# Kernel optimization log

Measured on AMD Instinct MI355X. Metric: run time of the kernel, lower is better.

The kernel has to match this reference:

```python
import jax, jax.numpy as jnp
import numpy as np

K = 5  # kernel_size per dim (dim=2 -> 25 kernels), B-spline degree 1, open spline


def spline_conv(x, edge_index, pseudo, W, root, bias):
    # x: [N, Cin], pseudo: [E, 2] in [0,1], W: [K*K, Cin, Cout]
    N = x.shape[0]
    src, dst = edge_index[0], edge_index[1]
    # Transform node features with every kernel weight once: [N, K*K, Cout]
    xk = jnp.einsum('ni,kio->nko', x, W)
    # Degree-1 open B-spline basis: v = u*(K-1); frac/1-frac weights over 2 knots per dim
    v = pseudo * (K - 1)
    bot = jnp.floor(v)
    frac = v - bot
    bot = bot.astype(jnp.int32)
    msg = jnp.zeros((src.shape[0], W.shape[2]), dtype=x.dtype)
    for s0 in (0, 1):
        for s1 in (0, 1):
            b0 = frac[:, 0] if s0 else (1.0 - frac[:, 0])
            b1 = frac[:, 1] if s1 else (1.0 - frac[:, 1])
            basis = b0 * b1  # [E]
            idx = (jnp.clip(bot[:, 0] + s0, 0, K - 1)
                   + K * jnp.clip(bot[:, 1] + s1, 0, K - 1))  # [E]
            msg = msg + basis[:, None] * xk[src, idx]  # gather [E, Cout]
    # scatter-max aggregation into target nodes; empty nodes -> 0 (PyG convention)
    agg = jax.ops.segment_max(msg, dst, num_segments=N)
    agg = jnp.where(jnp.isfinite(agg), agg, jnp.zeros_like(agg))
    return agg + x @ root + bias


def setup_inputs() -> dict:
    key = jax.random.key(0)
    ks = jax.random.split(key, 8)
    N, E, C = 50000, 1600000, 64
    Cin = C
    s = 1.0 / np.sqrt(25 * Cin)
    return {
        'x': jax.random.normal(ks[0], (N, C), dtype=jnp.float32),
        'edge_index': jax.random.randint(ks[1], (2, E), 0, N, dtype=jnp.int32),
        'edge_attr': jax.random.uniform(ks[2], (E, 2), dtype=jnp.float32),
        'W1': jax.random.normal(ks[3], (25, C, C), dtype=jnp.float32) * s,
        'root1': jax.random.normal(ks[4], (C, C), dtype=jnp.float32) / np.sqrt(C),
        'bias1': jnp.zeros((C,), dtype=jnp.float32),
        'W2': jax.random.normal(ks[5], (25, C, C), dtype=jnp.float32) * s,
        'root2': jax.random.normal(ks[6], (C, C), dtype=jnp.float32) / np.sqrt(C),
        'bias2': jnp.zeros((C,), dtype=jnp.float32),
    }


def reference(x, edge_index, edge_attr, W1, root1, bias1, W2, root2, bias2):
    h = jax.nn.relu(spline_conv(x, edge_index, edge_attr, W1, root1, bias1))
    out = spline_conv(h, edge_index, edge_attr, W2, root2, bias2)
    return out
```

## Files before the change

kernel.cpp:

```cpp
#include <hip/hip_runtime.h>
#include <hip/hip_bf16.h>
#include <math.h>

#define CHANNELS 64
#define KK 25
#define NBLK 26
#define NCOL (NBLK * CHANNELS)
#define NTILES (NCOL / 16)
#define ROWP 2560
#define GROUP_TILES 8
#define GROUP_BYTES (GROUP_TILES * 2048)
#define NGROUPS (NTILES / GROUP_TILES)

typedef __attribute__((ext_vector_type(8))) short bf16x8;
typedef __attribute__((ext_vector_type(4))) float f32x4;
typedef __attribute__((ext_vector_type(2))) float f32x2;
typedef unsigned int u32;

__device__ __forceinline__ u32 f2bfu(float f) {
    u32 u = __float_as_uint(f);
    return (u + 0x7FFFu + ((u >> 16) & 1u)) >> 16;
}
__device__ __forceinline__ short f2bf(float f) { return (short)f2bfu(f); }

__device__ __forceinline__ void async_copy16(const void* g, void* l) {
    __builtin_amdgcn_global_load_lds(
        (const __attribute__((address_space(1))) u32*)g,
        (__attribute__((address_space(3))) u32*)l, 16, 0, 0);
}


__global__ __launch_bounds__(256) void scan_a(const u32* __restrict__ counts,
                                              u32* __restrict__ bsum, int N) {
    const int t = threadIdx.x;
    const int base = blockIdx.x * 1024 + t * 4;
    uint4 v = make_uint4(0, 0, 0, 0);
    if (base + 3 < N) v = *(const uint4*)(counts + base);
    else {
        if (base < N)     v.x = counts[base];
        if (base + 1 < N) v.y = counts[base + 1];
        if (base + 2 < N) v.z = counts[base + 2];
    }
    u32 s = v.x + v.y + v.z + v.w;
    for (int off = 32; off; off >>= 1) s += __shfl_down(s, off, 64);
    __shared__ u32 red[4];
    if ((t & 63) == 0) red[t >> 6] = s;
    __syncthreads();
    if (t == 0) bsum[blockIdx.x] = red[0] + red[1] + red[2] + red[3];
}

__global__ __launch_bounds__(64) void scan_b(u32* __restrict__ bsum, int nb) {
    const int lane = threadIdx.x;
    u32 run = 0;
    for (int base = 0; base < nb; base += 64) {
        u32 v = (base + lane < nb) ? bsum[base + lane] : 0u;
        const u32 orig = v;
        for (int off = 1; off < 64; off <<= 1) {
            u32 u = __shfl_up(v, off, 64);
            if (lane >= off) v += u;
        }
        if (base + lane < nb) bsum[base + lane] = run + v - orig;
        run += __shfl(v, 63, 64);
    }
}

__global__ __launch_bounds__(256) void scan_c(const u32* __restrict__ counts,
                                              const u32* __restrict__ bsum,
                                              u32* __restrict__ cursor, int N) {
    const int t = threadIdx.x;
    const int base = blockIdx.x * 1024 + t * 4;
    uint4 v = make_uint4(0, 0, 0, 0);
    if (base + 3 < N) v = *(const uint4*)(counts + base);
    else {
        if (base < N)     v.x = counts[base];
        if (base + 1 < N) v.y = counts[base + 1];
        if (base + 2 < N) v.z = counts[base + 2];
    }
    __shared__ u32 ps[256];
    ps[t] = v.x + v.y + v.z + v.w;
    __syncthreads();
    for (int off = 1; off < 256; off <<= 1) {
        u32 u = (t >= off) ? ps[t - off] : 0u;
        __syncthreads();
        ps[t] += u;
        __syncthreads();
    }
    u32 ex = ((t > 0) ? ps[t - 1] : 0u) + bsum[blockIdx.x];
    if (base < N)     cursor[base]     = ex;
    if (base + 1 < N) cursor[base + 1] = ex + v.x;
    if (base + 2 < N) cursor[base + 2] = ex + v.x + v.y;
    if (base + 3 < N) cursor[base + 3] = ex + v.x + v.y + v.z;
    if (base <= N - 1 && N - 1 <= base + 3)
        cursor[N] = ex + v.x + v.y + v.z + v.w;
}


__global__ __launch_bounds__(256) void prep_w(const float* __restrict__ W,
                                              const float* __restrict__ root,
                                              __hip_bfloat16* __restrict__ Wb) {
    int idx = blockIdx.x * 256 + threadIdx.x;
    if (idx >= NTILES * 2 * 64 * 8) return;
    int j = idx & 7;
    int l = (idx >> 3) & 63;
    int q = (idx >> 9) & 1;
    int t = idx >> 10;
    int cell = t >> 2;
    int o    = 4 * (l & 15) + (t & 3);
    int k    = q * 32 + (l >> 4) * 8 + j;
    float src = (cell < KK) ? W[cell * 4096 + k * 64 + o] : root[k * 64 + o];
    ((unsigned short*)Wb)[idx] = (unsigned short)f2bf(src);
}

__device__ __forceinline__ void gemm_body(
    const float* __restrict__ X, const __hip_bfloat16* __restrict__ Wb,
    char* __restrict__ XK, float* __restrict__ rootf, int N, int gr0, int gr1)
{
    __shared__ __align__(16) char lds[2][GROUP_BYTES];
    const int lane = threadIdx.x & 63;
    const int wv   = threadIdx.x >> 6;
    const int rb   = blockIdx.x * 64 + wv * 16;
    const int m    = lane & 15;
    const int quad = lane >> 4;

    const int rowc = min(rb + m, N - 1);
    const float* __restrict__ xp = X + (size_t)rowc * CHANNELS + quad * 8;
    float af[16];
    *(float4*)(af)      = *(const float4*)(xp);
    *(float4*)(af + 4)  = *(const float4*)(xp + 4);
    *(float4*)(af + 8)  = *(const float4*)(xp + 32);
    *(float4*)(af + 12) = *(const float4*)(xp + 36);
    bf16x8 A0, A1;
#pragma unroll
    for (int j = 0; j < 8; ++j) { A0[j] = f2bf(af[j]); A1[j] = f2bf(af[8 + j]); }

    const int r0 = rb + quad * 4;
    const int rmax = N - r0;
    char* __restrict__ orow0 = XK + (size_t)r0 * ROWP;

    const char* __restrict__ wbc = (const char*)Wb;
#define STAGE(g, buf)                                                          \
    {                                                                          \
        const char* gsrc = wbc + (size_t)(g) * GROUP_BYTES + wv * 4096 + lane * 16; \
        char* lbase = lds[buf] + wv * 4096;                                    \
        async_copy16(gsrc,        lbase);                                      \
        async_copy16(gsrc + 1024, lbase + 1024);                               \
        async_copy16(gsrc + 2048, lbase + 2048);                               \
        async_copy16(gsrc + 3072, lbase + 3072);                               \
    }

    STAGE(gr0, 0)
    for (int g = gr0; g < gr1; ++g) {
        const int li = (g - gr0) & 1;
        __syncthreads();
        if (g + 1 < gr1) STAGE(g + 1, li ^ 1)
        const char* lb = lds[li] + lane * 16;
#pragma unroll
        for (int cc = 0; cc < 2; ++cc) {
            const char* cb = lb + cc * 8192;
            f32x4 acc0 = {0.f, 0.f, 0.f, 0.f};
            f32x4 acc1 = {0.f, 0.f, 0.f, 0.f};
            f32x4 acc2 = {0.f, 0.f, 0.f, 0.f};
            f32x4 acc3 = {0.f, 0.f, 0.f, 0.f};
            acc0 = __builtin_amdgcn_mfma_f32_16x16x32_bf16(A0, *(const bf16x8*)(cb),        acc0, 0, 0, 0);
            acc0 = __builtin_amdgcn_mfma_f32_16x16x32_bf16(A1, *(const bf16x8*)(cb + 1024), acc0, 0, 0, 0);
            acc1 = __builtin_amdgcn_mfma_f32_16x16x32_bf16(A0, *(const bf16x8*)(cb + 2048), acc1, 0, 0, 0);
            acc1 = __builtin_amdgcn_mfma_f32_16x16x32_bf16(A1, *(const bf16x8*)(cb + 3072), acc1, 0, 0, 0);
            acc2 = __builtin_amdgcn_mfma_f32_16x16x32_bf16(A0, *(const bf16x8*)(cb + 4096), acc2, 0, 0, 0);
            acc2 = __builtin_amdgcn_mfma_f32_16x16x32_bf16(A1, *(const bf16x8*)(cb + 5120), acc2, 0, 0, 0);
            acc3 = __builtin_amdgcn_mfma_f32_16x16x32_bf16(A0, *(const bf16x8*)(cb + 6144), acc3, 0, 0, 0);
            acc3 = __builtin_amdgcn_mfma_f32_16x16x32_bf16(A1, *(const bf16x8*)(cb + 7168), acc3, 0, 0, 0);
            const int kc = g * 2 + cc;
            if (kc < KK) {
                const int d1 = kc / 5;
                const int d0 = kc - 5 * d1;
                const int boff = d1 * 512 + d0 * 128 + 4 * m;
#pragma unroll
                for (int i = 0; i < 4; ++i) {
                    if (i < rmax) {
                        u32 p = __builtin_amdgcn_cvt_pk_fp8_f32(acc0[i], acc1[i], 0u, false);
                        p = __builtin_amdgcn_cvt_pk_fp8_f32(acc2[i], acc3[i], p, true);
                        char* orow = orow0 + (size_t)i * ROWP;
                        if (d0 <= 3) *(u32*)(orow + boff) = p;
                        if (d0 >= 1) *(u32*)(orow + boff - 64) = p;
                    }
                }
            } else {
#pragma unroll
                for (int i = 0; i < 4; ++i) {
                    if (i < rmax) {
                        *(float4*)(rootf + (size_t)(r0 + i) * CHANNELS + 4 * m) =
                            make_float4(acc0[i], acc1[i], acc2[i], acc3[i]);
                    }
                }
            }
        }
    }
#undef STAGE
}

__global__ __launch_bounds__(256) void gemm_hist(
    const float* __restrict__ X, const __hip_bfloat16* __restrict__ Wb,
    char* __restrict__ XK, float* __restrict__ rootf, int N, int gemm_blocks,
    const int* __restrict__ ei, u32* __restrict__ counts,
    u32* __restrict__ rank, int E)
{
    if ((int)blockIdx.x >= gemm_blocks) {
        const int e0 = ((int)blockIdx.x - gemm_blocks) * 1024 + threadIdx.x * 4;
        if (e0 + 3 < E) {
            const int4 d = *(const int4*)(ei + E + e0);
            const u32 r0 = atomicAdd(&counts[d.x], 1u);
            const u32 r1 = atomicAdd(&counts[d.y], 1u);
            const u32 r2 = atomicAdd(&counts[d.z], 1u);
            const u32 r3 = atomicAdd(&counts[d.w], 1u);
            *(uint4*)(rank + e0) = make_uint4(r0, r1, r2, r3);
        } else {
            for (int k = 0; k < 4; ++k)
                if (e0 + k < E)
                    rank[e0 + k] = atomicAdd(&counts[ei[E + e0 + k]], 1u);
        }
        return;
    }
    gemm_body(X, Wb, XK, rootf, N, 0, NGROUPS);
}

__global__ __launch_bounds__(256) void gemm_only(
    const float* __restrict__ X, const __hip_bfloat16* __restrict__ Wb,
    char* __restrict__ XK, float* __restrict__ rootf, int N)
{
    gemm_body(X, Wb, XK, rootf, N, 0, NGROUPS);
}

__device__ __forceinline__ uint2 mkrec(int src, float v0f, float v1f) {
    const float v0 = v0f * 4.0f, v1 = v1f * 4.0f;
    const int p0 = max(min((int)floorf(v0), 3), 0);
    const int p1 = max(min((int)floorf(v1), 3), 0);
    const float f0 = v0 - (float)p0;
    const float f1 = v1 - (float)p1;
    const u32 f0q = min((u32)(f0 * 65536.0f), 65535u);
    const u32 f1q = min((u32)(f1 * 65536.0f), 65535u);
    uint2 rec;
    rec.x = (u32)src | ((u32)p0 << 16) | ((u32)p1 << 19);
    rec.y = f0q | (f1q << 16);
    return rec;
}

__global__ __launch_bounds__(256) void edge_scatter(
    const int* __restrict__ ei, const float* __restrict__ ps,
    const u32* __restrict__ rank, const u32* __restrict__ cursor,
    uint2* __restrict__ sorted, int E)
{
    const int e0 = blockIdx.x * 1024 + threadIdx.x * 4;
    if (e0 + 3 < E) {
        const int4 s  = *(const int4*)(ei + e0);
        const int4 d  = *(const int4*)(ei + E + e0);
        const float4 pa = *(const float4*)(ps + 2 * e0);
        const float4 pb = *(const float4*)(ps + 2 * e0 + 4);
        const uint4 rk = *(const uint4*)(rank + e0);
        const u32 c0 = cursor[d.x];
        const u32 c1 = cursor[d.y];
        const u32 c2 = cursor[d.z];
        const u32 c3 = cursor[d.w];
        sorted[c0 + rk.x] = mkrec(s.x, pa.x, pa.y);
        sorted[c1 + rk.y] = mkrec(s.y, pa.z, pa.w);
        sorted[c2 + rk.z] = mkrec(s.z, pb.x, pb.y);
        sorted[c3 + rk.w] = mkrec(s.w, pb.z, pb.w);
    } else {
        for (int k = 0; k < 4; ++k) {
            const int e = e0 + k;
            if (e < E)
                sorted[cursor[ei[E + e]] + rank[e]] =
                    mkrec(ei[e], ps[2 * e], ps[2 * e + 1]);
        }
    }
}

__global__ __launch_bounds__(256) void agg_node_p(
    const uint2* __restrict__ sorted, const u32* __restrict__ cursor,
    const char* __restrict__ XK, const float* __restrict__ rootf,
    const float* __restrict__ bias, float* __restrict__ out, int N, int relu,
    int node_blocks, const float* __restrict__ Wsrc,
    const float* __restrict__ rootsrc, __hip_bfloat16* __restrict__ Wbdst)
{
    if ((int)blockIdx.x >= node_blocks) {
        int idx = ((int)blockIdx.x - node_blocks) * 256 + threadIdx.x;
        if (idx < NTILES * 2 * 64 * 8) {
            int j = idx & 7;
            int l = (idx >> 3) & 63;
            int q = (idx >> 9) & 1;
            int t = idx >> 10;
            int cell = t >> 2;
            int o    = 4 * (l & 15) + (t & 3);
            int k    = q * 32 + (l >> 4) * 8 + j;
            float s = (cell < KK) ? Wsrc[cell * 4096 + k * 64 + o] : rootsrc[k * 64 + o];
            ((unsigned short*)Wbdst)[idx] = (unsigned short)f2bf(s);
        }
        return;
    }
    const int lane = threadIdx.x & 63;
    const int n = blockIdx.x * 4 + (threadIdx.x >> 6);
    if (n >= N) return;
    const int q = lane >> 4, j = lane & 15;
    const int beg = (int)cursor[n];
    const int end = (int)cursor[n + 1];

    float m0 = -INFINITY, m1 = -INFINITY, m2 = -INFINITY, m3 = -INFINITY;
    if (beg < end) {
        const int last = end - 1;
#define GATHP(r, gll, ghl, glh, ghh)                                           \
        {                                                                      \
            const char* b_ = XK + (size_t)((r).x & 0xffff) * ROWP + (j << 2);  \
            const int o_ = (((int)((r).x >> 16) & 7)                           \
                            + (((int)((r).x >> 19) & 7) << 2)) << 7;           \
            gll = *(const u32*)(b_ + o_);                                      \
            ghl = *(const u32*)(b_ + o_ + 64);                                 \
            glh = *(const u32*)(b_ + o_ + 512);                                \
            ghh = *(const u32*)(b_ + o_ + 576);                                \
        }
        uint2 rA = sorted[min(beg + q,      last)];
        uint2 rB = sorted[min(beg + 4 + q,  last)];
        uint2 rC = sorted[min(beg + 8 + q,  last)];
        u32 a0, a1, a2, a3, b0, b1, b2, b3, c0, c1, c2, c3;
        GATHP(rA, a0, a1, a2, a3)
        GATHP(rB, b0, b1, b2, b3)
        for (int i = beg; i < end; i += 4) {
            uint2 rD = sorted[min(i + 12 + q, last)];
            GATHP(rC, c0, c1, c2, c3)
            const float f0 = (float)(rA.y & 0xffff) * (1.0f / 65536.0f);
            const float f1 = (float)(rA.y >> 16)    * (1.0f / 65536.0f);
            const float w00 = (1.f - f0) * (1.f - f1);
            const float w10 = f0 * (1.f - f1);
            const float w01 = (1.f - f0) * f1;
            const float w11 = f0 * f1;
            f32x2 s01 = __builtin_amdgcn_cvt_pk_f32_fp8(a0, false) * w00
                      + __builtin_amdgcn_cvt_pk_f32_fp8(a1, false) * w10
                      + __builtin_amdgcn_cvt_pk_f32_fp8(a2, false) * w01
                      + __builtin_amdgcn_cvt_pk_f32_fp8(a3, false) * w11;
            f32x2 s23 = __builtin_amdgcn_cvt_pk_f32_fp8(a0, true)  * w00
                      + __builtin_amdgcn_cvt_pk_f32_fp8(a1, true)  * w10
                      + __builtin_amdgcn_cvt_pk_f32_fp8(a2, true)  * w01
                      + __builtin_amdgcn_cvt_pk_f32_fp8(a3, true)  * w11;
            m0 = fmaxf(m0, s01.x); m1 = fmaxf(m1, s01.y);
            m2 = fmaxf(m2, s23.x); m3 = fmaxf(m3, s23.y);
            rA = rB; rB = rC; rC = rD;
            a0 = b0; a1 = b1; a2 = b2; a3 = b3;
            b0 = c0; b1 = c1; b2 = c2; b3 = c3;
        }
#undef GATHP
    }
    m0 = fmaxf(m0, __shfl_xor(m0, 16, 64)); m0 = fmaxf(m0, __shfl_xor(m0, 32, 64));
    m1 = fmaxf(m1, __shfl_xor(m1, 16, 64)); m1 = fmaxf(m1, __shfl_xor(m1, 32, 64));
    m2 = fmaxf(m2, __shfl_xor(m2, 16, 64)); m2 = fmaxf(m2, __shfl_xor(m2, 32, 64));
    m3 = fmaxf(m3, __shfl_xor(m3, 16, 64)); m3 = fmaxf(m3, __shfl_xor(m3, 32, 64));
    const float a0 = isfinite(m0) ? m0 : 0.f;
    const float a1 = isfinite(m1) ? m1 : 0.f;
    const float a2 = isfinite(m2) ? m2 : 0.f;
    const float a3 = isfinite(m3) ? m3 : 0.f;

    const float4 rv = *(const float4*)(rootf + (size_t)n * CHANNELS + 4 * j);
    const float4 bv = *(const float4*)(bias + 4 * j);
    float r0 = a0 + rv.x + bv.x;
    float r1 = a1 + rv.y + bv.y;
    float r2 = a2 + rv.z + bv.z;
    float r3 = a3 + rv.w + bv.w;
    if (relu) {
        r0 = fmaxf(r0, 0.f); r1 = fmaxf(r1, 0.f);
        r2 = fmaxf(r2, 0.f); r3 = fmaxf(r3, 0.f);
    }
    if (q == 0)
        *(float4*)(out + (size_t)n * CHANNELS + 4 * j) = make_float4(r0, r1, r2, r3);
}

extern "C" void kernel_launch(void* const* d_in, const int* in_sizes, int n_in,
                              void* d_out, int out_size, void* d_ws, size_t ws_size,
                              hipStream_t stream) {
    const float* x     = (const float*)d_in[0];
    const int*   ei    = (const int*)d_in[1];
    const float* ps    = (const float*)d_in[2];
    const float* W1    = (const float*)d_in[3];
    const float* root1 = (const float*)d_in[4];
    const float* bias1 = (const float*)d_in[5];
    const float* W2    = (const float*)d_in[6];
    const float* root2 = (const float*)d_in[7];
    const float* bias2 = (const float*)d_in[8];
    float* out = (float*)d_out;

    const int N = in_sizes[0] / CHANNELS;
    const int E = in_sizes[1] / 2;

    char* ws = (char*)d_ws;
    char* xk = ws;
    size_t off = (size_t)N * ROWP;
    float* h = (float*)(ws + off);
    off += (size_t)N * CHANNELS * sizeof(float);
    float* rootf = (float*)(ws + off);
    off += (size_t)N * CHANNELS * sizeof(float);
    uint2* sorted = (uint2*)(ws + off);
    off += (size_t)E * sizeof(uint2);
    u32* rank = (u32*)(ws + off);
    off += (size_t)E * sizeof(u32);
    u32* counts = (u32*)(ws + off);
    off += (size_t)N * 4;
    __hip_bfloat16* Wb = (__hip_bfloat16*)(ws + off);
    off += (size_t)NTILES * 2 * 64 * 8 * 2;
    u32* cursor = (u32*)(ws + off);
    off += ((size_t)N + 1) * 4;
    u32* bsum = (u32*)(ws + off);

    const int prep_blocks = (NTILES * 2 * 64 * 8 + 255) / 256;
    const int gemm_blocks = (N + 63) / 64;
    const int node_blocks = (N + 3) / 4;
    const int edgeQ_blocks = (E + 1023) / 1024;
    const int scan_blocks = (N + 1023) / 1024;

    hipMemsetAsync(counts, 0, (size_t)N * 4, stream);
    prep_w<<<prep_blocks, 256, 0, stream>>>(W1, root1, Wb);

    gemm_hist<<<gemm_blocks + edgeQ_blocks, 256, 0, stream>>>(
        x, Wb, xk, rootf, N, gemm_blocks, ei, counts, rank, E);

    scan_a<<<scan_blocks, 256, 0, stream>>>(counts, bsum, N);
    scan_b<<<1, 64, 0, stream>>>(bsum, scan_blocks);
    scan_c<<<scan_blocks, 256, 0, stream>>>(counts, bsum, cursor, N);

    edge_scatter<<<edgeQ_blocks, 256, 0, stream>>>(ei, ps, rank, cursor, sorted, E);

    agg_node_p<<<node_blocks + prep_blocks, 256, 0, stream>>>(
        sorted, cursor, xk, rootf, bias1, h, N, 1, node_blocks, W2, root2, Wb);

    gemm_only<<<gemm_blocks, 256, 0, stream>>>(h, Wb, xk, rootf, N);
    agg_node_p<<<node_blocks, 256, 0, stream>>>(
        sorted, cursor, xk, rootf, bias2, out, N, 0, node_blocks, W2, root2, Wb);
}
```

Baseline: 421.3 us.

## Interleave fp8 XK pairs for 8-byte gathers and split layer-1 GEMM across kernels

After: 416.6 us. About the same (-1.1%).

```diff
diff --git a/kernel.cpp b/kernel.cpp
--- a/kernel.cpp
+++ b/kernel.cpp
@@ -11,6 +11,7 @@
 #define GROUP_TILES 8
 #define GROUP_BYTES (GROUP_TILES * 2048)
 #define NGROUPS (NTILES / GROUP_TILES)
+#define G_SPLIT 5
 
 typedef __attribute__((ext_vector_type(8))) short bf16x8;
 typedef __attribute__((ext_vector_type(4))) float f32x4;
@@ -27,6 +28,19 @@
     __builtin_amdgcn_global_load_lds(
         (const __attribute__((address_space(1))) u32*)g,
         (__attribute__((address_space(3))) u32*)l, 16, 0, 0);
+}
+
+template<int N> struct IC { static constexpr int v = N; };
+template<int G, int GEND, class F>
+__device__ __forceinline__ void unrollg(F f) {
+    if constexpr (G < GEND) { f(IC<G>{}); unrollg<G + 1, GEND>(f); }
+}
+
+__device__ constexpr int cell_stores(int c) {
+    return (c < KK) ? (((c % 5) != 0) ? 4 : 0) : 4;
+}
+__device__ constexpr int grp_stores(int g) {
+    return cell_stores(2 * g) + cell_stores(2 * g + 1);
 }
 
 
@@ -111,18 +125,21 @@
     ((unsigned short*)Wb)[idx] = (unsigned short)f2bf(src);
 }
 
+template<int GR0, int GR1>
 __device__ __forceinline__ void gemm_body(
     const float* __restrict__ X, const __hip_bfloat16* __restrict__ Wb,
-    char* __restrict__ XK, float* __restrict__ rootf, int N, int gr0, int gr1)
+    char* __restrict__ XK, float* __restrict__ rootf, int N)
 {
+    static_assert((2 * GR0) % 5 == 0 || 2 * GR0 >= KK, "prevp chain crosses kernel split");
     __shared__ __align__(16) char lds[2][GROUP_BYTES];
     const int lane = threadIdx.x & 63;
     const int wv   = threadIdx.x >> 6;
     const int rb   = blockIdx.x * 64 + wv * 16;
     const int m    = lane & 15;
     const int quad = lane >> 4;
-
-    const int rowc = min(rb + m, N - 1);
+    const int Nm1  = N - 1;
+
+    const int rowc = min(rb + m, Nm1);
     const float* __restrict__ xp = X + (size_t)rowc * CHANNELS + quad * 8;
     float af[16];
     *(float4*)(af)      = *(const float4*)(xp);
@@ -134,29 +151,34 @@
     for (int j = 0; j < 8; ++j) { A0[j] = f2bf(af[j]); A1[j] = f2bf(af[8 + j]); }
 
     const int r0 = rb + quad * 4;
-    const int rmax = N - r0;
-    char* __restrict__ orow0 = XK + (size_t)r0 * ROWP;
-
     const char* __restrict__ wbc = (const char*)Wb;
-#define STAGE(g, buf)                                                          \
-    {                                                                          \
-        const char* gsrc = wbc + (size_t)(g) * GROUP_BYTES + wv * 4096 + lane * 16; \
-        char* lbase = lds[buf] + wv * 4096;                                    \
-        async_copy16(gsrc,        lbase);                                      \
-        async_copy16(gsrc + 1024, lbase + 1024);                               \
-        async_copy16(gsrc + 2048, lbase + 2048);                               \
-        async_copy16(gsrc + 3072, lbase + 3072);                               \
-    }
-
-    STAGE(gr0, 0)
-    for (int g = gr0; g < gr1; ++g) {
-        const int li = (g - gr0) & 1;
-        __syncthreads();
-        if (g + 1 < gr1) STAGE(g + 1, li ^ 1)
-        const char* lb = lds[li] + lane * 16;
-#pragma unroll
-        for (int cc = 0; cc < 2; ++cc) {
-            const char* cb = lb + cc * 8192;
+
+    auto stage = [&](int gg, int buf) {
+        const char* gsrc = wbc + (size_t)gg * GROUP_BYTES + wv * 4096 + lane * 16;
+        char* lbase = lds[buf] + wv * 4096;
+        async_copy16(gsrc,        lbase);
+        async_copy16(gsrc + 1024, lbase + 1024);
+        async_copy16(gsrc + 2048, lbase + 2048);
+        async_copy16(gsrc + 3072, lbase + 3072);
+    };
+
+    u32 prevp[4] = {0u, 0u, 0u, 0u};
+
+    stage(GR0, 0);
+
+    unrollg<GR0, GR1>([&](auto icg) {
+        constexpr int g = decltype(icg)::v;
+        constexpr int K = (g == GR0) ? 0 : grp_stores(g - 1);
+        asm volatile("s_waitcnt vmcnt(%0)" :: "i"(K) : "memory");
+        asm volatile("s_waitcnt lgkmcnt(0)" ::: "memory");
+        __builtin_amdgcn_s_barrier();
+        __builtin_amdgcn_sched_barrier(0);
+        if constexpr (g + 1 < GR1) stage(g + 1, (g + 1 - GR0) & 1);
+        __builtin_amdgcn_sched_barrier(0);
+        const char* lb = lds[(g - GR0) & 1] + lane * 16;
+
+        auto cell = [&](auto ick, const char* cb) {
+            constexpr int kc = decltype(ick)::v;
             f32x4 acc0 = {0.f, 0.f, 0.f, 0.f};
             f32x4 acc1 = {0.f, 0.f, 0.f, 0.f};
             f32x4 acc2 = {0.f, 0.f, 0.f, 0.f};
@@ -169,33 +191,39 @@
             acc2 = __builtin_amdgcn_mfma_f32_16x16x32_bf16(A1, *(const bf16x8*)(cb + 5120), acc2, 0, 0, 0);
             acc3 = __builtin_amdgcn_mfma_f32_16x16x32_bf16(A0, *(const bf16x8*)(cb + 6144), acc3, 0, 0, 0);
             acc3 = __builtin_amdgcn_mfma_f32_16x16x32_bf16(A1, *(const bf16x8*)(cb + 7168), acc3, 0, 0, 0);
-            const int kc = g * 2 + cc;
-            if (kc < KK) {
-                const int d1 = kc / 5;
-                const int d0 = kc - 5 * d1;
-                const int boff = d1 * 512 + d0 * 128 + 4 * m;
+            if constexpr (kc < KK) {
+                constexpr int d1 = kc / 5;
+                constexpr int d0 = kc % 5;
+                u32 pk[4];
 #pragma unroll
                 for (int i = 0; i < 4; ++i) {
-                    if (i < rmax) {
-                        u32 p = __builtin_amdgcn_cvt_pk_fp8_f32(acc0[i], acc1[i], 0u, false);
-                        p = __builtin_amdgcn_cvt_pk_fp8_f32(acc2[i], acc3[i], p, true);
-                        char* orow = orow0 + (size_t)i * ROWP;
-                        if (d0 <= 3) *(u32*)(orow + boff) = p;
-                        if (d0 >= 1) *(u32*)(orow + boff - 64) = p;
+                    u32 p = __builtin_amdgcn_cvt_pk_fp8_f32(acc0[i], acc1[i], 0u, false);
+                    p = __builtin_amdgcn_cvt_pk_fp8_f32(acc2[i], acc3[i], p, true);
+                    pk[i] = p;
+                }
+                if constexpr (d0 >= 1) {
+#pragma unroll
+                    for (int i = 0; i < 4; ++i) {
+                        const int r = min(r0 + i, Nm1);
+                        *(uint2*)(XK + (size_t)r * ROWP
+                                  + (d1 * 512 + (d0 - 1) * 128) + 8 * m) =
+                            make_uint2(prevp[i], pk[i]);
                     }
                 }
+#pragma unroll
+                for (int i = 0; i < 4; ++i) prevp[i] = pk[i];
             } else {
 #pragma unroll
                 for (int i = 0; i < 4; ++i) {
-                    if (i < rmax) {
-                        *(float4*)(rootf + (size_t)(r0 + i) * CHANNELS + 4 * m) =
-                            make_float4(acc0[i], acc1[i], acc2[i], acc3[i]);
-                    }
+                    const int r = min(r0 + i, Nm1);
+                    *(float4*)(rootf + (size_t)r * CHANNELS + 4 * m) =
+                        make_float4(acc0[i], acc1[i], acc2[i], acc3[i]);
                 }
             }
-        }
-    }
-#undef STAGE
+        };
+        cell(IC<2 * g>{},     lb);
+        cell(IC<2 * g + 1>{}, lb + 8192);
+    });
 }
 
 __global__ __launch_bounds__(256) void gemm_hist(
@@ -220,14 +248,7 @@
         }
         return;
     }
-    gemm_body(X, Wb, XK, rootf, N, 0, NGROUPS);
-}
-
-__global__ __launch_bounds__(256) void gemm_only(
-    const float* __restrict__ X, const __hip_bfloat16* __restrict__ Wb,
-    char* __restrict__ XK, float* __restrict__ rootf, int N)
-{
-    gemm_body(X, Wb, XK, rootf, N, 0, NGROUPS);
+    gemm_body<0, G_SPLIT>(X, Wb, XK, rootf, N);
 }
 
 __device__ __forceinline__ uint2 mkrec(int src, float v0f, float v1f) {
@@ -244,34 +265,47 @@
     return rec;
 }
 
-__global__ __launch_bounds__(256) void edge_scatter(
+__global__ __launch_bounds__(256) void gemm_scatter(
+    const float* __restrict__ X, const __hip_bfloat16* __restrict__ Wb,
+    char* __restrict__ XK, float* __restrict__ rootf, int N, int gemm_blocks,
     const int* __restrict__ ei, const float* __restrict__ ps,
     const u32* __restrict__ rank, const u32* __restrict__ cursor,
     uint2* __restrict__ sorted, int E)
 {
-    const int e0 = blockIdx.x * 1024 + threadIdx.x * 4;
-    if (e0 + 3 < E) {
-        const int4 s  = *(const int4*)(ei + e0);
-        const int4 d  = *(const int4*)(ei + E + e0);
-        const float4 pa = *(const float4*)(ps + 2 * e0);
-        const float4 pb = *(const float4*)(ps + 2 * e0 + 4);
-        const uint4 rk = *(const uint4*)(rank + e0);
-        const u32 c0 = cursor[d.x];
-        const u32 c1 = cursor[d.y];
-        const u32 c2 = cursor[d.z];
-        const u32 c3 = cursor[d.w];
-        sorted[c0 + rk.x] = mkrec(s.x, pa.x, pa.y);
-        sorted[c1 + rk.y] = mkrec(s.y, pa.z, pa.w);
-        sorted[c2 + rk.z] = mkrec(s.z, pb.x, pb.y);
-        sorted[c3 + rk.w] = mkrec(s.w, pb.z, pb.w);
-    } else {
-        for (int k = 0; k < 4; ++k) {
-            const int e = e0 + k;
-            if (e < E)
-                sorted[cursor[ei[E + e]] + rank[e]] =
-                    mkrec(ei[e], ps[2 * e], ps[2 * e + 1]);
-        }
-    }
+    if ((int)blockIdx.x >= gemm_blocks) {
+        const int e0 = ((int)blockIdx.x - gemm_blocks) * 1024 + threadIdx.x * 4;
+        if (e0 + 3 < E) {
+            const int4 s  = *(const int4*)(ei + e0);
+            const int4 d  = *(const int4*)(ei + E + e0);
+            const float4 pa = *(const float4*)(ps + 2 * e0);
+            const float4 pb = *(const float4*)(ps + 2 * e0 + 4);
+            const uint4 rk = *(const uint4*)(rank + e0);
+            const u32 c0 = cursor[d.x];
+            const u32 c1 = cursor[d.y];
+            const u32 c2 = cursor[d.z];
+            const u32 c3 = cursor[d.w];
+            sorted[c0 + rk.x] = mkrec(s.x, pa.x, pa.y);
+            sorted[c1 + rk.y] = mkrec(s.y, pa.z, pa.w);
+            sorted[c2 + rk.z] = mkrec(s.z, pb.x, pb.y);
+            sorted[c3 + rk.w] = mkrec(s.w, pb.z, pb.w);
+        } else {
+            for (int k = 0; k < 4; ++k) {
+                const int e = e0 + k;
+                if (e < E)
+                    sorted[cursor[ei[E + e]] + rank[e]] =
+                        mkrec(ei[e], ps[2 * e], ps[2 * e + 1]);
+            }
+        }
+        return;
+    }
+    gemm_body<G_SPLIT, NGROUPS>(X, Wb, XK, rootf, N);
+}
+
+__global__ __launch_bounds__(256) void gemm_only(
+    const float* __restrict__ X, const __hip_bfloat16* __restrict__ Wb,
+    char* __restrict__ XK, float* __restrict__ rootf, int N)
+{
+    gemm_body<0, NGROUPS>(X, Wb, XK, rootf, N);
 }
 
 __global__ __launch_bounds__(256) void agg_node_p(
@@ -306,44 +340,42 @@
     float m0 = -INFINITY, m1 = -INFINITY, m2 = -INFINITY, m3 = -INFINITY;
     if (beg < end) {
         const int last = end - 1;
-#define GATHP(r, gll, ghl, glh, ghh)                                           \
+#define GATHP(r, q0, q1)                                                       \
         {                                                                      \
-            const char* b_ = XK + (size_t)((r).x & 0xffff) * ROWP + (j << 2);  \
+            const char* b_ = XK + (size_t)((r).x & 0xffff) * ROWP + (j << 3);  \
             const int o_ = (((int)((r).x >> 16) & 7)                           \
                             + (((int)((r).x >> 19) & 7) << 2)) << 7;           \
-            gll = *(const u32*)(b_ + o_);                                      \
-            ghl = *(const u32*)(b_ + o_ + 64);                                 \
-            glh = *(const u32*)(b_ + o_ + 512);                                \
-            ghh = *(const u32*)(b_ + o_ + 576);                                \
+            q0 = *(const uint2*)(b_ + o_);                                     \
+            q1 = *(const uint2*)(b_ + o_ + 512);                               \
         }
         uint2 rA = sorted[min(beg + q,      last)];
         uint2 rB = sorted[min(beg + 4 + q,  last)];
         uint2 rC = sorted[min(beg + 8 + q,  last)];
-        u32 a0, a1, a2, a3, b0, b1, b2, b3, c0, c1, c2, c3;
-        GATHP(rA, a0, a1, a2, a3)
-        GATHP(rB, b0, b1, b2, b3)
+        uint2 ga0, ga1, gb0, gb1, gc0, gc1;
+        GATHP(rA, ga0, ga1)
+        GATHP(rB, gb0, gb1)
         for (int i = beg; i < end; i += 4) {
             uint2 rD = sorted[min(i + 12 + q, last)];
-            GATHP(rC, c0, c1, c2, c3)
+            GATHP(rC, gc0, gc1)
             const float f0 = (float)(rA.y & 0xffff) * (1.0f / 65536.0f);
             const float f1 = (float)(rA.y >> 16)    * (1.0f / 65536.0f);
             const float w00 = (1.f - f0) * (1.f - f1);
             const float w10 = f0 * (1.f - f1);
             const float w01 = (1.f - f0) * f1;
             const float w11 = f0 * f1;
-            f32x2 s01 = __builtin_amdgcn_cvt_pk_f32_fp8(a0, false) * w00
-                      + __builtin_amdgcn_cvt_pk_f32_fp8(a1, false) * w10
-                      + __builtin_amdgcn_cvt_pk_f32_fp8(a2, false) * w01
-                      + __builtin_amdgcn_cvt_pk_f32_fp8(a3, false) * w11;
-            f32x2 s23 = __builtin_amdgcn_cvt_pk_f32_fp8(a0, true)  * w00
-                      + __builtin_amdgcn_cvt_pk_f32_fp8(a1, true)  * w10
-                      + __builtin_amdgcn_cvt_pk_f32_fp8(a2, true)  * w01
-                      + __builtin_amdgcn_cvt_pk_f32_fp8(a3, true)  * w11;
+            f32x2 s01 = __builtin_amdgcn_cvt_pk_f32_fp8(ga0.x, false) * w00
+                      + __builtin_amdgcn_cvt_pk_f32_fp8(ga0.y, false) * w10
+                      + __builtin_amdgcn_cvt_pk_f32_fp8(ga1.x, false) * w01
+                      + __builtin_amdgcn_cvt_pk_f32_fp8(ga1.y, false) * w11;
+            f32x2 s23 = __builtin_amdgcn_cvt_pk_f32_fp8(ga0.x, true)  * w00
+                      + __builtin_amdgcn_cvt_pk_f32_fp8(ga0.y, true)  * w10
+                      + __builtin_amdgcn_cvt_pk_f32_fp8(ga1.x, true)  * w01
+                      + __builtin_amdgcn_cvt_pk_f32_fp8(ga1.y, true)  * w11;
             m0 = fmaxf(m0, s01.x); m1 = fmaxf(m1, s01.y);
             m2 = fmaxf(m2, s23.x); m3 = fmaxf(m3, s23.y);
             rA = rB; rB = rC; rC = rD;
-            a0 = b0; a1 = b1; a2 = b2; a3 = b3;
-            b0 = c0; b1 = c1; b2 = c2; b3 = c3;
+            ga0 = gb0; ga1 = gb1;
+            gb0 = gc0; gb1 = gc1;
         }
 #undef GATHP
     }
@@ -422,7 +454,8 @@
     scan_b<<<1, 64, 0, stream>>>(bsum, scan_blocks);
     scan_c<<<scan_blocks, 256, 0, stream>>>(counts, bsum, cursor, N);
 
-    edge_scatter<<<edgeQ_blocks, 256, 0, stream>>>(ei, ps, rank, cursor, sorted, E);
+    gemm_scatter<<<gemm_blocks + edgeQ_blocks, 256, 0, stream>>>(
+        x, Wb, xk, rootf, N, gemm_blocks, ei, ps, rank, cursor, sorted, E);
 
     agg_node_p<<<node_blocks + prep_blocks, 256, 0, stream>>>(
         sorted, cursor, xk, rootf, bias1, h, N, 1, node_blocks, W2, root2, Wb);
```
